# Kernel tuning notes

Measured on AMD Instinct MI355X. Metric: run time of the kernel, lower is better.

## Reference

```python
import jax, jax.numpy as jnp
import numpy as np

H = 1024   # hidden size
E = 8      # num experts
B, S = 4, 2048


def setup_inputs() -> dict:
    key = jax.random.key(0)
    k1, k2, k3, k4 = jax.random.split(key, 4)
    x = jax.random.normal(k1, (B, S, H), dtype=jnp.float32)
    wg = jax.random.normal(k2, (H, E), dtype=jnp.float32) * 0.02      # gate weight
    W = jax.random.normal(k3, (E, H, H), dtype=jnp.float32) * 0.02    # expert Linear weights (out, in) per expert
    b = jax.random.normal(k4, (E, H), dtype=jnp.float32) * 0.02       # expert Linear biases
    return {"x": x, "wg": wg, "W": W, "b": b}


def reference(x, wg, W, b):
    Bb, Ss, Hh = x.shape
    Ee = wg.shape[1]
    T = Bb * Ss
    C = T // Ee  # capacity (capacity_factor = 1.0, top-1)

    xt = x.reshape(T, Hh)
    logits = xt @ wg                                   # [T, E]
    probs = jax.nn.softmax(logits, axis=-1)            # [T, E]
    idx = jnp.argmax(probs, axis=-1)                   # [T] top-1 expert
    mask = jax.nn.one_hot(idx, Ee, dtype=xt.dtype)     # [T, E]

    # position of each token within its expert's queue (0-based)
    locations = jnp.cumsum(mask, axis=0) - mask        # [T, E]
    # drop tokens over capacity
    mask = mask * (locations < C).astype(xt.dtype)
    gate = jnp.sum(probs * mask, axis=-1)              # [T] gate prob (0 if dropped)
    loc_s = jnp.sum(locations * mask, axis=-1).astype(jnp.int32)  # [T]
    loc_oh = jax.nn.one_hot(loc_s, C, dtype=xt.dtype)  # [T, C]

    dispatch = mask[:, :, None] * loc_oh[:, None, :]   # [T, E, C]
    combine = gate[:, None, None] * dispatch           # [T, E, C]

    # dispatch tokens -> per-expert buffers [E, C, H]
    exp_in = jnp.einsum('tec,th->ech', dispatch, xt)
    # per-expert Linear: y = x @ W_e^T + b_e
    exp_out = jnp.einsum('ech,efh->ecf', exp_in, W) + b[:, None, :]
    # combine back to tokens, scaled by gate prob
    out = jnp.einsum('tec,ecf->tf', combine, exp_out)  # [T, H]
    return out.reshape(Bb, Ss, Hh)
```

## Files before the change

### kernel.cpp

```cpp
#include <hip/hip_runtime.h>

#define H 1024
#define E 8
#define T 8192
#define CAP 1024

typedef __bf16 bf16x8 __attribute__((ext_vector_type(8)));
typedef float  f32x4  __attribute__((ext_vector_type(4)));
typedef unsigned short u16;

__device__ __forceinline__ u16 f2bf(float f) {
    union { float f; unsigned u; } v; v.f = f;
    unsigned r = v.u + 0x7FFFu + ((v.u >> 16) & 1u);
    return (u16)(r >> 16);
}

__device__ __forceinline__ unsigned cvt2bf(float lo, float hi) {
    unsigned r;
    asm("v_cvt_pk_bf16_f32 %0, %1, %2" : "=v"(r) : "v"(lo), "v"(hi));
    return r;
}

typedef __attribute__((address_space(1))) const void* gas_t;
typedef __attribute__((address_space(3))) void* las_t;
__device__ __forceinline__ void gld16(const void* g, void* l) {
    __builtin_amdgcn_global_load_lds((gas_t)g, (las_t)l, 16, 0, 0);
}

__global__ __launch_bounds__(256) void gate_kernel(
    const float* __restrict__ x, const float* __restrict__ wg,
    int* __restrict__ eid, float* __restrict__ gate, u16* __restrict__ xbf) {
    const int tid = threadIdx.x;
    const int wv = tid >> 6, lane = tid & 63;
    const int tbase = blockIdx.x * 16 + wv * 4;
    const int h00 = lane * 4;

    float a[4][8];
    #pragma unroll
    for (int j = 0; j < 4; ++j)
        #pragma unroll
        for (int e = 0; e < 8; ++e) a[j][e] = 0.f;

    #pragma unroll
    for (int q = 0; q < 4; ++q) {
        const int h0 = q * 256 + h00;
        float4 xv[4];
        #pragma unroll
        for (int j = 0; j < 4; ++j)
            xv[j] = *(const float4*)(x + (size_t)(tbase + j) * H + h0);
        #pragma unroll
        for (int j = 0; j < 4; ++j) {
            ushort4 o;
            o.x = f2bf(xv[j].x); o.y = f2bf(xv[j].y);
            o.z = f2bf(xv[j].z); o.w = f2bf(xv[j].w);
            *(ushort4*)(xbf + (size_t)(tbase + j) * H + h0) = o;
        }
        float wr[4][8];
        #pragma unroll
        for (int r = 0; r < 4; ++r) {
            const float4* p = (const float4*)(wg + (size_t)(h0 + r) * E);
            float4 lo = p[0], hi = p[1];
            wr[r][0] = lo.x; wr[r][1] = lo.y; wr[r][2] = lo.z; wr[r][3] = lo.w;
            wr[r][4] = hi.x; wr[r][5] = hi.y; wr[r][6] = hi.z; wr[r][7] = hi.w;
        }
        #pragma unroll
        for (int e = 0; e < 8; ++e)
            #pragma unroll
            for (int j = 0; j < 4; ++j)
                a[j][e] += xv[j].x * wr[0][e] + xv[j].y * wr[1][e]
                         + xv[j].z * wr[2][e] + xv[j].w * wr[3][e];
    }

    const bool b0 = lane & 1, b1 = lane & 2, b2 = lane & 4;
    const int elane = ((lane & 1) << 2) | (lane & 2) | ((lane >> 2) & 1);

    #pragma unroll
    for (int j = 0; j < 4; ++j) {
        float* A = a[j];
        #pragma unroll
        for (int k = 0; k < 4; ++k) {
            float t = b0 ? A[k] : A[k + 4];
            t = __shfl_xor(t, 1);
            A[k] = (b0 ? A[k + 4] : A[k]) + t;
        }
        #pragma unroll
        for (int k = 0; k < 2; ++k) {
            float t = b1 ? A[k] : A[k + 2];
            t = __shfl_xor(t, 2);
            A[k] = (b1 ? A[k + 2] : A[k]) + t;
        }
        {
            float t = b2 ? A[0] : A[1];
            t = __shfl_xor(t, 4);
            A[0] = (b2 ? A[1] : A[0]) + t;
        }
        float v = A[0];
        v += __shfl_xor(v, 8); v += __shfl_xor(v, 16); v += __shfl_xor(v, 32);
        float m = v; int mi = elane;
        #pragma unroll
        for (int off = 1; off <= 4; off <<= 1) {
            float om = __shfl_xor(m, off);
            int   oi = __shfl_xor(mi, off);
            if (om > m || (om == m && oi < mi)) { m = om; mi = oi; }
        }
        float s = expf(v - m);
        s += __shfl_xor(s, 1); s += __shfl_xor(s, 2); s += __shfl_xor(s, 4);
        if (lane == 0) {
            eid[tbase + j]  = mi;
            gate[tbase + j] = 1.0f / s;
        }
    }
}

#define SCAN_T 1024
#define STPT 8
__global__ __launch_bounds__(1024) void scan_kernel(
    const int* __restrict__ eid, float* __restrict__ gate,
    int* __restrict__ perm) {
    __shared__ int cnt[SCAN_T][E];
    __shared__ int part[E][32];
    const int tid = threadIdx.x;

    for (int i = tid; i < E * CAP; i += SCAN_T) perm[i] = -1;

    const int t0 = tid * STPT;
    int ei[STPT];
    #pragma unroll
    for (int i = 0; i < STPT; ++i) ei[i] = eid[t0 + i];

    int c[E];
    #pragma unroll
    for (int e = 0; e < E; ++e) c[e] = 0;
    #pragma unroll
    for (int i = 0; i < STPT; ++i)
        #pragma unroll
        for (int e = 0; e < E; ++e) c[e] += (ei[i] == e);
    #pragma unroll
    for (int e = 0; e < E; ++e) cnt[tid][e] = c[e];
    __syncthreads();

    if (tid < 256) {
        const int e = tid >> 5, g = tid & 31;
        int s = 0;
        for (int i = g * 32; i < g * 32 + 32; ++i) s += cnt[i][e];
        part[e][g] = s;
    }
    __syncthreads();
    if (tid < E) {
        int run = 0;
        #pragma unroll
        for (int g = 0; g < 32; ++g) { int v = part[tid][g]; part[tid][g] = run; run += v; }
    }
    __syncthreads();
    if (tid < 256) {
        const int e = tid >> 5, g = tid & 31;
        int run = part[e][g];
        for (int i = g * 32; i < g * 32 + 32; ++i) { int v = cnt[i][e]; cnt[i][e] = run; run += v; }
    }
    __syncthreads();

    #pragma unroll
    for (int e = 0; e < E; ++e) c[e] = cnt[tid][e];
    #pragma unroll
    for (int i = 0; i < STPT; ++i) {
        const int t = t0 + i, e0 = ei[i];
        int pos = 0;
        #pragma unroll
        for (int k = 0; k < E; ++k) if (e0 == k) pos = c[k]++;
        if (pos < CAP) perm[e0 * CAP + pos] = t;
        else gate[t] = 0.f;
    }
}

__global__ __launch_bounds__(512, 4) void moe_gemm_bf(
    const u16* __restrict__ xbf, const float* __restrict__ W,
    const float* __restrict__ bias, const int* __restrict__ perm,
    const float* __restrict__ gate, float* __restrict__ out) {
    __shared__ __align__(16) u16 As[2][128 * 64];
    __shared__ __align__(16) u16 Bs[2][128 * 64];
    __shared__ int   perm_s[128];
    __shared__ float gate_s[128];

    const int tid = threadIdx.x;
    const int bid = blockIdx.x;

    if (bid < 64) {
        const int t = bid * 128 + (tid >> 2);
        if (gate[t] == 0.f) {
            const int part = tid & 3;
            float4 z = make_float4(0.f, 0.f, 0.f, 0.f);
            float4* o = (float4*)(out + (size_t)t * H + part * 256);
            #pragma unroll
            for (int i = 0; i < 64; ++i) o[i] = z;
        }
        return;
    }

    const int idx = bid - 64;
    const int fb = idx >> 6;
    const int mb = (idx >> 3) & 7;
    const int e  = idx & 7;

    if (tid < 128) {
        const int t = perm[e * CAP + mb * 128 + tid];
        perm_s[tid] = t;
        gate_s[tid] = (t >= 0) ? gate[t] : 0.f;
    }
    __syncthreads();

    const int lane = tid & 63;
    const int wv = tid >> 6;
    const int wm = wv >> 2;
    const int wn = wv & 3;
    const int l16 = lane & 15, quad = lane >> 4;

    const int rl  = lane >> 3;
    const int cch = lane & 7;
    const int gch = cch ^ rl;
    const u16*   ga[2];
    const float* gb[2];
    #pragma unroll
    for (int q = 0; q < 2; ++q) {
        const int r = wv * 16 + q * 8 + rl;
        const int tA = perm_s[r];
        const int tok = tA >= 0 ? tA : 0;
        ga[q] = xbf + (size_t)tok * H + gch * 8;
        gb[q] = W + (size_t)e * H * H + (size_t)(fb * 128 + r) * H + gch * 8;
    }

    f32x4 acc[4][2] = {};

    {
        float4 nb[2][2];
        #pragma unroll
        for (int q = 0; q < 2; ++q) {
            const float4* p = (const float4*)gb[q];
            nb[q][0] = p[0]; nb[q][1] = p[1];
        }
        #pragma unroll
        for (int q = 0; q < 2; ++q)
            gld16(ga[q], &As[0][(wv * 16 + q * 8) * 64 + lane * 8]);
        #pragma unroll
        for (int q = 0; q < 2; ++q) {
            uint4 v;
            v.x = cvt2bf(nb[q][0].x, nb[q][0].y); v.y = cvt2bf(nb[q][0].z, nb[q][0].w);
            v.z = cvt2bf(nb[q][1].x, nb[q][1].y); v.w = cvt2bf(nb[q][1].z, nb[q][1].w);
            *(uint4*)&Bs[0][(wv * 16 + q * 8 + rl) * 64 + cch * 8] = v;
        }
        #pragma unroll
        for (int q = 0; q < 2; ++q) { ga[q] += 64; gb[q] += 64; }
    }
    __syncthreads();

#define STEP(CUR, NXT, PF)                                                    \
    {                                                                         \
        float4 nb[2][2];                                                      \
        if (PF) {                                                             \
            _Pragma("unroll")                                                 \
            for (int q = 0; q < 2; ++q) {                                     \
                const float4* p = (const float4*)gb[q];                       \
                nb[q][0] = p[0]; nb[q][1] = p[1];                             \
            }                                                                 \
            _Pragma("unroll")                                                 \
            for (int q = 0; q < 2; ++q)                                       \
                gld16(ga[q], &As[NXT][(wv * 16 + q * 8) * 64 + lane * 8]);    \
        }                                                                     \
        _Pragma("unroll")                                                     \
        for (int s = 0; s < 2; ++s) {                                         \
            bf16x8 af[4], bfr[2];                                             \
            const int cc = (s * 4 + quad) ^ (l16 & 7);                        \
            _Pragma("unroll")                                                 \
            for (int i = 0; i < 4; ++i)                                       \
                af[i] = *(const bf16x8*)&As[CUR][(wm * 64 + i * 16 + l16) * 64 + cc * 8]; \
            _Pragma("unroll")                                                 \
            for (int i = 0; i < 2; ++i)                                       \
                bfr[i] = *(const bf16x8*)&Bs[CUR][(wn * 32 + i * 16 + l16) * 64 + cc * 8]; \
            _Pragma("unroll")                                                 \
            for (int mi = 0; mi < 4; ++mi)                                    \
                _Pragma("unroll")                                             \
                for (int ni = 0; ni < 2; ++ni)                                \
                    acc[mi][ni] = __builtin_amdgcn_mfma_f32_16x16x32_bf16(    \
                        af[mi], bfr[ni], acc[mi][ni], 0, 0, 0);               \
        }                                                                     \
        if (PF) {                                                             \
            _Pragma("unroll")                                                 \
            for (int q = 0; q < 2; ++q) {                                     \
                uint4 v;                                                      \
                v.x = cvt2bf(nb[q][0].x, nb[q][0].y); v.y = cvt2bf(nb[q][0].z, nb[q][0].w); \
                v.z = cvt2bf(nb[q][1].x, nb[q][1].y); v.w = cvt2bf(nb[q][1].z, nb[q][1].w); \
                *(uint4*)&Bs[NXT][(wv * 16 + q * 8 + rl) * 64 + cch * 8] = v; \
            }                                                                 \
            _Pragma("unroll")                                                 \
            for (int q = 0; q < 2; ++q) { ga[q] += 64; gb[q] += 64; }         \
        }                                                                     \
        __syncthreads();                                                      \
    }

    for (int kt2 = 0; kt2 < 7; ++kt2) {
        STEP(0, 1, true)
        STEP(1, 0, true)
    }
    STEP(0, 1, true)
    STEP(1, 0, false)
#undef STEP

    float bv[2];
    #pragma unroll
    for (int ni = 0; ni < 2; ++ni)
        bv[ni] = bias[e * H + fb * 128 + wn * 32 + ni * 16 + l16];

    #pragma unroll
    for (int mi = 0; mi < 4; ++mi) {
        #pragma unroll
        for (int r = 0; r < 4; ++r) {
            const int rowl = wm * 64 + mi * 16 + quad * 4 + r;
            const int t = perm_s[rowl];
            if (t < 0) continue;
            const float g = gate_s[rowl];
            float* orow = out + (size_t)t * H + fb * 128 + wn * 32;
            #pragma unroll
            for (int ni = 0; ni < 2; ++ni)
                orow[ni * 16 + l16] = g * (acc[mi][ni][r] + bv[ni]);
        }
    }
}

extern "C" void kernel_launch(void* const* d_in, const int* in_sizes, int n_in,
                              void* d_out, int out_size, void* d_ws, size_t ws_size,
                              hipStream_t stream) {
    const float* x    = (const float*)d_in[0];
    const float* wg   = (const float*)d_in[1];
    const float* W    = (const float*)d_in[2];
    const float* bias = (const float*)d_in[3];
    float* out = (float*)d_out;

    int*   eid  = (int*)d_ws;
    float* gate = (float*)((char*)d_ws + (size_t)T * 4);
    int*   perm = (int*)((char*)d_ws + (size_t)T * 8);
    u16*   xbf  = (u16*)((char*)d_ws + (size_t)T * 12);

    gate_kernel<<<T / 16, 256, 0, stream>>>(x, wg, eid, gate, xbf);
    scan_kernel<<<1, SCAN_T, 0, stream>>>(eid, gate, perm);
    moe_gemm_bf<<<64 + 512, 512, 0, stream>>>(xbf, W, bias, perm, gate, out);
}
```

Before: 165.3 us.

## Pre-convert expert weights to bf16 and use a 256x128 tile with three-stage direct-to-LDS pipeline

Expert weight conversion from fp32 to bf16 moves into extra blocks of the gate kernel, writing a bf16 copy to workspace. The GEMM can then load both A and B straight into LDS with global_load_lds, with no per-step register conversion. The GEMM tile grows to 256 tokens by 128 outputs, with a triple-buffered LDS pipeline and explicit vmcnt waits plus barriers, so the grid drops from 512 to 256 GEMM blocks. In exchange, every call adds a 32MB fp32 read and 16MB bf16 write of W, and the larger tile lowers occupancy and the block count.

```diff
diff --git a/kernel.cpp b/kernel.cpp
--- a/kernel.cpp
+++ b/kernel.cpp
@@ -15,22 +15,35 @@
     return (u16)(r >> 16);
 }
 
-__device__ __forceinline__ unsigned cvt2bf(float lo, float hi) {
-    unsigned r;
-    asm("v_cvt_pk_bf16_f32 %0, %1, %2" : "=v"(r) : "v"(lo), "v"(hi));
-    return r;
-}
-
 typedef __attribute__((address_space(1))) const void* gas_t;
 typedef __attribute__((address_space(3))) void* las_t;
 __device__ __forceinline__ void gld16(const void* g, void* l) {
     __builtin_amdgcn_global_load_lds((gas_t)g, (las_t)l, 16, 0, 0);
 }
 
-__global__ __launch_bounds__(256) void gate_kernel(
+#define GATE_BLOCKS 512
+#define CVT_BLOCKS  1536
+
+__global__ __launch_bounds__(256) void gatecvt_kernel(
     const float* __restrict__ x, const float* __restrict__ wg,
-    int* __restrict__ eid, float* __restrict__ gate, u16* __restrict__ xbf) {
+    const float* __restrict__ W,
+    int* __restrict__ eid, float* __restrict__ gate,
+    u16* __restrict__ xbf, u16* __restrict__ Wbf) {
     const int tid = threadIdx.x;
+
+    if (blockIdx.x >= GATE_BLOCKS) {
+        int i = (blockIdx.x - GATE_BLOCKS) * 256 + tid;
+        const int n4 = E * H * H / 4;
+        const int stride = CVT_BLOCKS * 256;
+        for (; i < n4; i += stride) {
+            float4 v = ((const float4*)W)[i];
+            ushort4 o;
+            o.x = f2bf(v.x); o.y = f2bf(v.y); o.z = f2bf(v.z); o.w = f2bf(v.w);
+            ((ushort4*)Wbf)[i] = o;
+        }
+        return;
+    }
+
     const int wv = tid >> 6, lane = tid & 63;
     const int tbase = blockIdx.x * 16 + wv * 4;
     const int h00 = lane * 4;
@@ -172,20 +185,20 @@
     }
 }
 
-__global__ __launch_bounds__(512, 4) void moe_gemm_bf(
-    const u16* __restrict__ xbf, const float* __restrict__ W,
+__global__ __launch_bounds__(512, 2) void moe_gemm_bf(
+    const u16* __restrict__ xbf, const u16* __restrict__ Wbf,
     const float* __restrict__ bias, const int* __restrict__ perm,
     const float* __restrict__ gate, float* __restrict__ out) {
-    __shared__ __align__(16) u16 As[2][128 * 64];
-    __shared__ __align__(16) u16 Bs[2][128 * 64];
-    __shared__ int   perm_s[128];
-    __shared__ float gate_s[128];
+    __shared__ __align__(16) u16 As[3][256 * 64];
+    __shared__ __align__(16) u16 Bs[3][128 * 64];
+    __shared__ int   perm_s[256];
+    __shared__ float gate_s[256];
 
     const int tid = threadIdx.x;
     const int bid = blockIdx.x;
 
-    if (bid < 64) {
-        const int t = bid * 128 + (tid >> 2);
+    if (bid >= 256) {
+        const int t = (bid - 256) * 128 + (tid >> 2);
         if (gate[t] == 0.f) {
             const int part = tid & 3;
             float4 z = make_float4(0.f, 0.f, 0.f, 0.f);
@@ -196,13 +209,12 @@
         return;
     }
 
-    const int idx = bid - 64;
-    const int fb = idx >> 6;
-    const int mb = (idx >> 3) & 7;
-    const int e  = idx & 7;
-
-    if (tid < 128) {
-        const int t = perm[e * CAP + mb * 128 + tid];
+    const int e  = bid & 7;
+    const int mb = (bid >> 3) & 3;
+    const int fb = bid >> 5;
+
+    if (tid < 256) {
+        const int t = perm[e * CAP + mb * 256 + tid];
         perm_s[tid] = t;
         gate_s[tid] = (t >= 0) ? gate[t] : 0.f;
     }
@@ -210,116 +222,103 @@
 
     const int lane = tid & 63;
     const int wv = tid >> 6;
-    const int wm = wv >> 2;
-    const int wn = wv & 3;
+    const int wm2 = wv >> 1;
+    const int wn2 = wv & 1;
     const int l16 = lane & 15, quad = lane >> 4;
 
     const int rl  = lane >> 3;
     const int cch = lane & 7;
     const int gch = cch ^ rl;
-    const u16*   ga[2];
-    const float* gb[2];
-    #pragma unroll
-    for (int q = 0; q < 2; ++q) {
-        const int r = wv * 16 + q * 8 + rl;
+
+    const u16* ga[4];
+    #pragma unroll
+    for (int q = 0; q < 4; ++q) {
+        const int r = q * 64 + wv * 8 + rl;
         const int tA = perm_s[r];
         const int tok = tA >= 0 ? tA : 0;
         ga[q] = xbf + (size_t)tok * H + gch * 8;
-        gb[q] = W + (size_t)e * H * H + (size_t)(fb * 128 + r) * H + gch * 8;
-    }
-
-    f32x4 acc[4][2] = {};
-
-    {
-        float4 nb[2][2];
-        #pragma unroll
-        for (int q = 0; q < 2; ++q) {
-            const float4* p = (const float4*)gb[q];
-            nb[q][0] = p[0]; nb[q][1] = p[1];
-        }
-        #pragma unroll
-        for (int q = 0; q < 2; ++q)
-            gld16(ga[q], &As[0][(wv * 16 + q * 8) * 64 + lane * 8]);
-        #pragma unroll
-        for (int q = 0; q < 2; ++q) {
-            uint4 v;
-            v.x = cvt2bf(nb[q][0].x, nb[q][0].y); v.y = cvt2bf(nb[q][0].z, nb[q][0].w);
-            v.z = cvt2bf(nb[q][1].x, nb[q][1].y); v.w = cvt2bf(nb[q][1].z, nb[q][1].w);
-            *(uint4*)&Bs[0][(wv * 16 + q * 8 + rl) * 64 + cch * 8] = v;
-        }
-        #pragma unroll
-        for (int q = 0; q < 2; ++q) { ga[q] += 64; gb[q] += 64; }
-    }
-    __syncthreads();
-
-#define STEP(CUR, NXT, PF)                                                    \
+    }
+    const u16* gb[2];
+    #pragma unroll
+    for (int q = 0; q < 2; ++q) {
+        const int r = fb * 128 + q * 64 + wv * 8 + rl;
+        gb[q] = Wbf + (size_t)e * H * H + (size_t)r * H + gch * 8;
+    }
+
+#define STAGE(BUF, TT)                                                        \
     {                                                                         \
-        float4 nb[2][2];                                                      \
-        if (PF) {                                                             \
-            _Pragma("unroll")                                                 \
-            for (int q = 0; q < 2; ++q) {                                     \
-                const float4* p = (const float4*)gb[q];                       \
-                nb[q][0] = p[0]; nb[q][1] = p[1];                             \
-            }                                                                 \
-            _Pragma("unroll")                                                 \
-            for (int q = 0; q < 2; ++q)                                       \
-                gld16(ga[q], &As[NXT][(wv * 16 + q * 8) * 64 + lane * 8]);    \
-        }                                                                     \
         _Pragma("unroll")                                                     \
-        for (int s = 0; s < 2; ++s) {                                         \
-            bf16x8 af[4], bfr[2];                                             \
-            const int cc = (s * 4 + quad) ^ (l16 & 7);                        \
-            _Pragma("unroll")                                                 \
-            for (int i = 0; i < 4; ++i)                                       \
-                af[i] = *(const bf16x8*)&As[CUR][(wm * 64 + i * 16 + l16) * 64 + cc * 8]; \
-            _Pragma("unroll")                                                 \
-            for (int i = 0; i < 2; ++i)                                       \
-                bfr[i] = *(const bf16x8*)&Bs[CUR][(wn * 32 + i * 16 + l16) * 64 + cc * 8]; \
-            _Pragma("unroll")                                                 \
-            for (int mi = 0; mi < 4; ++mi)                                    \
-                _Pragma("unroll")                                             \
-                for (int ni = 0; ni < 2; ++ni)                                \
-                    acc[mi][ni] = __builtin_amdgcn_mfma_f32_16x16x32_bf16(    \
-                        af[mi], bfr[ni], acc[mi][ni], 0, 0, 0);               \
-        }                                                                     \
-        if (PF) {                                                             \
-            _Pragma("unroll")                                                 \
-            for (int q = 0; q < 2; ++q) {                                     \
-                uint4 v;                                                      \
-                v.x = cvt2bf(nb[q][0].x, nb[q][0].y); v.y = cvt2bf(nb[q][0].z, nb[q][0].w); \
-                v.z = cvt2bf(nb[q][1].x, nb[q][1].y); v.w = cvt2bf(nb[q][1].z, nb[q][1].w); \
-                *(uint4*)&Bs[NXT][(wv * 16 + q * 8 + rl) * 64 + cch * 8] = v; \
-            }                                                                 \
-            _Pragma("unroll")                                                 \
-            for (int q = 0; q < 2; ++q) { ga[q] += 64; gb[q] += 64; }         \
-        }                                                                     \
-        __syncthreads();                                                      \
-    }
-
-    for (int kt2 = 0; kt2 < 7; ++kt2) {
-        STEP(0, 1, true)
-        STEP(1, 0, true)
-    }
-    STEP(0, 1, true)
-    STEP(1, 0, false)
-#undef STEP
-
-    float bv[2];
-    #pragma unroll
-    for (int ni = 0; ni < 2; ++ni)
-        bv[ni] = bias[e * H + fb * 128 + wn * 32 + ni * 16 + l16];
+        for (int q = 0; q < 4; ++q)                                           \
+            gld16(ga[q] + (TT) * 64, &As[BUF][(q * 64 + wv * 8) * 64 + lane * 8]); \
+        _Pragma("unroll")                                                     \
+        for (int q = 0; q < 2; ++q)                                           \
+            gld16(gb[q] + (TT) * 64, &Bs[BUF][(q * 64 + wv * 8) * 64 + lane * 8]); \
+    }
+
+    f32x4 acc[4][4] = {};
+
+    STAGE(0, 0)
+    STAGE(1, 1)
+    STAGE(2, 2)
+    asm volatile("s_waitcnt vmcnt(12)" ::: "memory");
+    __builtin_amdgcn_sched_barrier(0);
+    __builtin_amdgcn_s_barrier();
+
+    int cur = 0;
+    for (int t = 0; t < 16; ++t) {
+        const u16* cA = As[cur];
+        const u16* cB = Bs[cur];
+        #pragma unroll
+        for (int kh = 0; kh < 2; ++kh) {
+            bf16x8 af[4], bf[4];
+            const int cc = (kh * 4 + quad) ^ (l16 & 7);
+            #pragma unroll
+            for (int mi = 0; mi < 4; ++mi)
+                af[mi] = *(const bf16x8*)&cA[(wm2 * 64 + mi * 16 + l16) * 64 + cc * 8];
+            #pragma unroll
+            for (int ni = 0; ni < 4; ++ni)
+                bf[ni] = *(const bf16x8*)&cB[(wn2 * 64 + ni * 16 + l16) * 64 + cc * 8];
+            #pragma unroll
+            for (int mi = 0; mi < 4; ++mi)
+                #pragma unroll
+                for (int ni = 0; ni < 4; ++ni)
+                    acc[mi][ni] = __builtin_amdgcn_mfma_f32_16x16x32_bf16(
+                        af[mi], bf[ni], acc[mi][ni], 0, 0, 0);
+        }
+        if (t == 15) break;
+
+        __builtin_amdgcn_sched_barrier(0);
+        __builtin_amdgcn_s_barrier();
+        if (t < 13) {
+            STAGE(cur, t + 3)
+            asm volatile("s_waitcnt vmcnt(12)" ::: "memory");
+        } else if (t == 13) {
+            asm volatile("s_waitcnt vmcnt(6)" ::: "memory");
+        } else {
+            asm volatile("s_waitcnt vmcnt(0)" ::: "memory");
+        }
+        __builtin_amdgcn_sched_barrier(0);
+        __builtin_amdgcn_s_barrier();
+        cur = (cur == 2) ? 0 : cur + 1;
+    }
+#undef STAGE
+
+    float bv[4];
+    #pragma unroll
+    for (int ni = 0; ni < 4; ++ni)
+        bv[ni] = bias[e * H + fb * 128 + wn2 * 64 + ni * 16 + l16];
 
     #pragma unroll
     for (int mi = 0; mi < 4; ++mi) {
         #pragma unroll
         for (int r = 0; r < 4; ++r) {
-            const int rowl = wm * 64 + mi * 16 + quad * 4 + r;
+            const int rowl = wm2 * 64 + mi * 16 + quad * 4 + r;
             const int t = perm_s[rowl];
             if (t < 0) continue;
             const float g = gate_s[rowl];
-            float* orow = out + (size_t)t * H + fb * 128 + wn * 32;
-            #pragma unroll
-            for (int ni = 0; ni < 2; ++ni)
+            float* orow = out + (size_t)t * H + fb * 128 + wn2 * 64;
+            #pragma unroll
+            for (int ni = 0; ni < 4; ++ni)
                 orow[ni * 16 + l16] = g * (acc[mi][ni][r] + bv[ni]);
         }
     }
@@ -338,8 +337,10 @@
     float* gate = (float*)((char*)d_ws + (size_t)T * 4);
     int*   perm = (int*)((char*)d_ws + (size_t)T * 8);
     u16*   xbf  = (u16*)((char*)d_ws + (size_t)T * 12);
-
-    gate_kernel<<<T / 16, 256, 0, stream>>>(x, wg, eid, gate, xbf);
+    u16*   Wbf  = xbf + (size_t)T * H;
+
+    gatecvt_kernel<<<GATE_BLOCKS + CVT_BLOCKS, 256, 0, stream>>>(
+        x, wg, W, eid, gate, xbf, Wbf);
     scan_kernel<<<1, SCAN_T, 0, stream>>>(eid, gate, perm);
-    moe_gemm_bf<<<64 + 512, 512, 0, stream>>>(xbf, W, bias, perm, gate, out);
-}
+    moe_gemm_bf<<<256 + 64, 512, 0, stream>>>(xbf, Wbf, bias, perm, gate, out);
+}
```

Result: faster. 158.6 us (-4.0%).
